# Performance work log

Measured on AMD Instinct MI355X. Metric: run time of the kernel, lower is better.

Reference implementation:

```python
import jax, jax.numpy as jnp
import numpy as np
import math

CHUNK = 128


def setup_inputs() -> dict:
    key = jax.random.key(0)
    ks = jax.random.split(key, 12)
    B, S, H, D = 2, 4096, 1024, 2048  # D = hidden_dim * expansion_factor
    std = 0.02
    inp = {
        "hidden_states": jax.random.normal(ks[0], (B, S, H), jnp.float32),
        "Wq": jax.random.normal(ks[1], (H, D), jnp.float32) * std,
        "bq": jnp.zeros((D,), jnp.float32),
        "Wk": jax.random.normal(ks[2], (H, D), jnp.float32) * std,
        "bk": jnp.zeros((D,), jnp.float32),
        "Wv": jax.random.normal(ks[3], (H, D), jnp.float32) * std,
        "bv": jnp.zeros((D,), jnp.float32),
        "Wg": jax.random.normal(ks[4], (H, D), jnp.float32) * std,
        "bg": jnp.zeros((D,), jnp.float32),
        "Wo": jax.random.normal(ks[5], (D, H), jnp.float32) * std,
        "bo": jnp.zeros((H,), jnp.float32),
    }
    return inp


def reference(hidden_states, Wq, bq, Wk, bk, Wv, bv, Wg, bg, Wo, bo):
    B, S, H = hidden_states.shape
    D = Wq.shape[1]
    cs = CHUNK
    nC = S // cs  # seq_len chosen as multiple of chunk_size (no padding path)

    q = hidden_states @ Wq + bq
    k = hidden_states @ Wk + bk
    v = hidden_states @ Wv + bv
    gate = jax.nn.sigmoid(hidden_states @ Wg + bg)

    qc = q.reshape(B, nC, cs, D)
    kc = k.reshape(B, nC, cs, D)
    vc = v.reshape(B, nC, cs, D)
    gc = gate.reshape(B, nC, cs, D)

    # intra-chunk causal softmax attention (vectorized over all chunks)
    scale = 1.0 / math.sqrt(D)
    attn = jnp.einsum('bncd,bnkd->bnck', qc, kc) * scale  # [B,nC,cs,cs]
    causal = jnp.tril(jnp.ones((cs, cs), bool))
    attn = jnp.where(causal, attn, -jnp.inf)
    attn = jax.nn.softmax(attn, axis=-1)
    local = jnp.einsum('bnck,bnkd->bncd', attn, vc)

    # inter-chunk linear-attention state accumulation:
    # cross_i = q_i @ sum_{j<i} K_j^T V_j  (sequential scan over chunks)
    def step(state, xs):
        qi, ki, vi = xs  # each [B,cs,D]
        cross = jnp.einsum('bcd,bde->bce', qi, state)
        state = state + jnp.einsum('bcd,bce->bde', ki, vi)
        return state, cross

    state0 = jnp.zeros((B, D, D), hidden_states.dtype)
    _, cross = jax.lax.scan(
        step, state0,
        (qc.transpose(1, 0, 2, 3), kc.transpose(1, 0, 2, 3), vc.transpose(1, 0, 2, 3)))
    cross = cross.transpose(1, 0, 2, 3)  # [B,nC,cs,D]

    out = (local + cross) * gc
    out = out.reshape(B, S, D)
    return out @ Wo + bo
```

## Files before the change

kernel.cpp:

```cpp
#include <hip/hip_runtime.h>
#include <hip/hip_bf16.h>
#include <math.h>


typedef __bf16 bf16_t;
typedef __bf16 bf16x8 __attribute__((ext_vector_type(8)));
typedef __bf16 bf16x4 __attribute__((ext_vector_type(4)));
typedef float f32x4 __attribute__((ext_vector_type(4)));

#define NB_ 2
#define SEQ 4096
#define HID 1024
#define DD 2048
#define BS 8192
#define LDS_BIG 73728
#define LDS_PAIR 49152

__device__ __forceinline__ void async16(const void* g, void* l) {
  __builtin_amdgcn_global_load_lds(
      (const __attribute__((address_space(1))) void*)g,
      (__attribute__((address_space(3))) void*)l, 16, 0, 0);
}

#define VMW0 asm volatile("s_waitcnt vmcnt(0)" ::: "memory")
#define BARR __builtin_amdgcn_s_barrier()
#define FEN asm volatile("" ::: "memory")

template <int WM, int WN>
__device__ __forceinline__ void coreTB(const bf16_t* __restrict__ A, int lda,
                                       const bf16_t* __restrict__ B, int ldb, int nt,
                                       bf16_t* lds, f32x4 (&acc)[4][4]) {
  constexpr int T = WM * WN * 64;
  constexpr int AE = WM * 64 * 32;
  constexpr int BUF = AE + WN * 64 * 32;
  constexpr int NISS = BUF / (T * 8);
  const int t = threadIdx.x;
  const int lane = t & 63, w = t >> 6;
  const int wm = w / WN, wn = w % WN;
  const int lr = lane & 15, lg = lane >> 4;

  int aOff[4], bOff[4];
#pragma unroll
  for (int f = 0; f < 4; ++f) {
    int ra = wm * 64 + f * 16 + lr;
    aOff[f] = ra * 32 + (((lg + (ra >> 1)) & 3) << 3);
    int rb = wn * 64 + f * 16 + lr;
    bOff[f] = AE + rb * 32 + (((lg + (rb >> 1)) & 3) << 3);
  }
  int src[NISS];
#pragma unroll
  for (int q = 0; q < NISS; ++q) {
    int e = q * T * 8 + t * 8;
    bool isB = (q * T * 8) >= AE;
    int e2 = isB ? e - AE : e;
    int r = e2 >> 5;
    int g = (((e2 >> 3) & 3) - (r >> 1)) & 3;
    src[q] = r * (isB ? ldb : lda) + g * 8;
  }
#pragma unroll
  for (int m = 0; m < 4; ++m)
#pragma unroll
    for (int n = 0; n < 4; ++n) acc[m][n] = (f32x4){0.f, 0.f, 0.f, 0.f};

#pragma unroll
  for (int q = 0; q < NISS; ++q) {
    bool isB = (q * T * 8) >= AE;
    async16((isB ? B : A) + src[q], lds + q * T * 8 + t * 8);
  }
  {
    const int k1 = (1 < nt ? 1 : 0) << 5;
#pragma unroll
    for (int q = 0; q < NISS; ++q) {
      bool isB = (q * T * 8) >= AE;
      async16((isB ? B : A) + k1 + src[q], lds + BUF + q * T * 8 + t * 8);
    }
  }

  for (int tt = 0; tt < nt; ++tt) {
    bf16_t* cur = lds + (tt % 3) * BUF;
    bf16_t* nxt = lds + ((tt + 2) % 3) * BUF;
    const int kn = (tt + 2 < nt ? tt + 2 : 0) << 5;
    if constexpr (NISS == 3) {
      asm volatile("s_waitcnt vmcnt(3)" ::: "memory");
    } else if constexpr (NISS == 4) {
      asm volatile("s_waitcnt vmcnt(4)" ::: "memory");
    } else {
      asm volatile("s_waitcnt vmcnt(0)" ::: "memory");
    }
    BARR; FEN;
    bf16x8 af[4], bv[4];
#pragma unroll
    for (int f = 0; f < 4; ++f) af[f] = *reinterpret_cast<const bf16x8*>(&cur[aOff[f]]);
#pragma unroll
    for (int f = 0; f < 4; ++f) bv[f] = *reinterpret_cast<const bf16x8*>(&cur[bOff[f]]);
#pragma unroll
    for (int q = 0; q < NISS; ++q) {
      bool isB = (q * T * 8) >= AE;
      async16((isB ? B : A) + kn + src[q], nxt + q * T * 8 + t * 8);
    }
    __builtin_amdgcn_s_setprio(1);
#pragma unroll
    for (int mf = 0; mf < 4; ++mf)
#pragma unroll
      for (int nf = 0; nf < 4; ++nf)
        acc[mf][nf] =
            __builtin_amdgcn_mfma_f32_16x16x32_bf16(af[mf], bv[nf], acc[mf][nf], 0, 0, 0);
    __builtin_amdgcn_s_setprio(0);
  }
  VMW0;
  BARR; FEN;
}

__global__ void k_cvt(const float4* __restrict__ in, bf16x4* __restrict__ out, int n4) {
  int i = blockIdx.x * blockDim.x + threadIdx.x;
  if (i < n4) {
    float4 v = in[i];
    bf16x4 o;
    o[0] = (bf16_t)v.x; o[1] = (bf16_t)v.y; o[2] = (bf16_t)v.z; o[3] = (bf16_t)v.w;
    out[i] = o;
  }
}

__global__ void k_tconv(const float* __restrict__ in, bf16_t* __restrict__ out,
                        int R, int C) {
  __shared__ bf16_t tile[64][65];
  int bc = blockIdx.x, br = blockIdx.y;
  int t = threadIdx.x;
  int c = t & 63, r0 = t >> 6;
#pragma unroll
  for (int rr = 0; rr < 64; rr += 4) {
    int r = rr + r0;
    tile[r][c] = (bf16_t)in[(long)(br * 64 + r) * C + bc * 64 + c];
  }
  __syncthreads();
#pragma unroll
  for (int rr = 0; rr < 64; rr += 4) {
    int r = rr + r0;
    out[(long)(bc * 64 + r) * R + br * 64 + c] = tile[c][r];
  }
}

__global__ __launch_bounds__(512, 4) void k_gemm_qkvg(
    const bf16_t* __restrict__ hsb, const bf16_t* __restrict__ Wt4,
    const float* __restrict__ bq, const float* __restrict__ bk,
    const float* __restrict__ bv, const float* __restrict__ bg,
    bf16_t* __restrict__ out, bf16_t* __restrict__ Vt) {
  extern __shared__ bf16_t lds[];
  const int SP = 136;
  const int SPT = 264;
  int i = blockIdx.x;
  int xcd = i & 7, g = i >> 3;
  int mb = g >> 3;
  int nb = xcd * 8 + (g & 7);
  f32x4 acc[4][4];
  coreTB<4, 2>(hsb + (long)mb * 256 * HID, HID, Wt4 + (long)nb * 128 * HID, HID,
               HID / 32, lds, acc);
  const int t = threadIdx.x, lane = t & 63, w = t >> 6;
  const int wm = w >> 1, wn = w & 1, lr = lane & 15, lg = lane >> 4;
  int z = nb >> 4;
  const float* bias = z == 0 ? bq : z == 1 ? bk : z == 2 ? bv : bg;
  int colT = (nb & 15) * 128;
  float b4[4];
#pragma unroll
  for (int nf = 0; nf < 4; ++nf) b4[nf] = bias[colT + wn * 64 + nf * 16 + lr];
  if (z != 2) {
#pragma unroll
    for (int mf = 0; mf < 4; ++mf)
#pragma unroll
      for (int reg = 0; reg < 4; ++reg) {
        int lrow = wm * 64 + mf * 16 + lg * 4 + reg;
#pragma unroll
        for (int nf = 0; nf < 4; ++nf) {
          float v = acc[mf][nf][reg] + b4[nf];
          if (z == 3) v = 1.f / (1.f + __expf(-v));
          lds[lrow * SP + wn * 64 + nf * 16 + lr] = (bf16_t)v;
        }
      }
    __syncthreads();
    bf16_t* O = out + (long)z * BS * DD + (long)mb * 256 * DD + colT;
#pragma unroll
    for (int it = 0; it < 8; ++it) {
      int s = it * 512 + t;
      int row = s >> 4, sg = s & 15;
      bf16x8 v = *reinterpret_cast<const bf16x8*>(&lds[row * SP + sg * 8]);
      *reinterpret_cast<bf16x8*>(&O[(long)row * DD + sg * 8]) = v;
    }
  } else {
#pragma unroll
    for (int mf = 0; mf < 4; ++mf)
#pragma unroll
      for (int reg = 0; reg < 4; ++reg) {
        int lrow = wm * 64 + mf * 16 + lg * 4 + reg;
#pragma unroll
        for (int nf = 0; nf < 4; ++nf) {
          int d = wn * 64 + nf * 16 + lr;
          lds[d * SPT + lrow] = (bf16_t)(acc[mf][nf][reg] + b4[nf]);
        }
      }
    __syncthreads();
    int bz = mb >> 4, smb = mb & 15;
    bf16_t* Vd = Vt + ((long)bz * DD + colT) * SEQ + smb * 256;
#pragma unroll
    for (int it = 0; it < 8; ++it) {
      int s = it * 512 + t;
      int d = s >> 5, sg = s & 31;
      bf16x8 v = *reinterpret_cast<const bf16x8*>(&lds[d * SPT + sg * 8]);
      *reinterpret_cast<bf16x8*>(&Vd[(long)d * SEQ + sg * 8]) = v;
    }
  }
}

__global__ __launch_bounds__(256, 3) void k_pair(const bf16_t* __restrict__ Q,
                                                 const bf16_t* __restrict__ Kb,
                                                 bf16_t* __restrict__ P) {
  extern __shared__ bf16_t lds[];
  const int SP = 136;
  int p = blockIdx.x, b = blockIdx.y;
  int c = 0, base = 0;
  while (base + c + 1 <= p) { base += c + 1; ++c; }
  int jt = p - base;
  f32x4 acc[4][4];
  coreTB<2, 2>(Q + ((long)b * SEQ + (long)c * 128) * DD, DD,
               Kb + ((long)b * SEQ + (long)jt * 128) * DD, DD, DD / 32, lds, acc);
  const int t = threadIdx.x, lane = t & 63, w = t >> 6;
  const int wm = w >> 1, wn = w & 1, lr = lane & 15, lg = lane >> 4;
  bf16_t* Pt = P + ((long)b * SEQ + (long)c * 128) * (long)SEQ + (long)jt * 128;
  const bool diag = (jt == c);
  const float scale = 0.02209708691207961f;
#pragma unroll
  for (int mf = 0; mf < 4; ++mf)
#pragma unroll
    for (int reg = 0; reg < 4; ++reg) {
      int row = wm * 64 + mf * 16 + lg * 4 + reg;
#pragma unroll
      for (int nf = 0; nf < 4; ++nf) {
        int col = wn * 64 + nf * 16 + lr;
        float v = acc[mf][nf][reg];
        if (diag) v = (col <= row) ? v * scale : -1e30f;
        lds[row * SP + col] = (bf16_t)v;
      }
    }
  __syncthreads();
  if (diag) {
    if (t < 128) {
      int r = t;
      bf16_t* rowp = lds + r * SP;
      float mx = -1e30f;
      for (int cc = 0; cc <= r; ++cc) mx = fmaxf(mx, (float)rowp[cc]);
      float ssum = 0.f;
      for (int cc = 0; cc <= r; ++cc) ssum += __expf((float)rowp[cc] - mx);
      float inv = 1.f / ssum;
      for (int cc = 0; cc < 128; ++cc) {
        float v = (cc <= r) ? __expf((float)rowp[cc] - mx) * inv : 0.f;
        rowp[cc] = (bf16_t)v;
      }
    }
    __syncthreads();
  }
#pragma unroll
  for (int it = 0; it < 8; ++it) {
    int s = it * 256 + t;
    int row = s >> 4, sg = s & 15;
    bf16x8 v = *reinterpret_cast<const bf16x8*>(&lds[row * SP + sg * 8]);
    *reinterpret_cast<bf16x8*>(&Pt[(long)row * SEQ + sg * 8]) = v;
  }
  if (diag && !(c & 1)) {
    bf16x8 zv = {};
#pragma unroll
    for (int it = 0; it < 8; ++it) {
      int s = it * 256 + t;
      int row = s >> 4, sg = s & 15;
      *reinterpret_cast<bf16x8*>(&Pt[(long)row * SEQ + 128 + sg * 8]) = zv;
    }
  }
}

__global__ __launch_bounds__(512, 4) void k_gemm2(const bf16_t* __restrict__ P,
                                                  const bf16_t* __restrict__ Vt,
                                                  const bf16_t* __restrict__ G,
                                                  bf16_t* __restrict__ OutPre) {
  extern __shared__ bf16_t lds[];
  const int SP = 136;
  int bid = blockIdx.x;
  int ip = 15 - (bid >> 5);
  int r2 = bid & 31;
  int nb = r2 >> 1, b2 = r2 & 1;
  f32x4 acc[4][4];
  coreTB<4, 2>(P + ((long)b2 * SEQ + (long)ip * 256) * (long)SEQ, SEQ,
               Vt + (long)b2 * DD * SEQ + (long)nb * 128 * SEQ, SEQ, (ip + 1) * 8,
               lds, acc);
  const int t = threadIdx.x, lane = t & 63, w = t >> 6;
  const int wm = w >> 1, wn = w & 1, lr = lane & 15, lg = lane >> 4;
  long rowb = (long)b2 * SEQ + (long)ip * 256;
#pragma unroll
  for (int mf = 0; mf < 4; ++mf)
#pragma unroll
    for (int reg = 0; reg < 4; ++reg) {
      int lrow = wm * 64 + mf * 16 + lg * 4 + reg;
#pragma unroll
      for (int nf = 0; nf < 4; ++nf) {
        int col = wn * 64 + nf * 16 + lr;
        float gg = (float)G[(rowb + lrow) * DD + nb * 128 + col];
        lds[lrow * SP + col] = (bf16_t)(acc[mf][nf][reg] * gg);
      }
    }
  __syncthreads();
  bf16_t* O = OutPre + rowb * DD + nb * 128;
#pragma unroll
  for (int it = 0; it < 8; ++it) {
    int s = it * 512 + t;
    int row = s >> 4, sg = s & 15;
    bf16x8 v = *reinterpret_cast<const bf16x8*>(&lds[row * SP + sg * 8]);
    *reinterpret_cast<bf16x8*>(&O[(long)row * DD + sg * 8]) = v;
  }
}

__global__ __launch_bounds__(512, 4) void k_gemm3(const bf16_t* __restrict__ OutPre,
                                                  const bf16_t* __restrict__ Wot,
                                                  const float* __restrict__ bo,
                                                  float* __restrict__ out) {
  extern __shared__ bf16_t lds[];
  int mb = blockIdx.x >> 2, nb = blockIdx.x & 3;
  f32x4 acc[4][4];
  coreTB<2, 4>(OutPre + (long)mb * 128 * DD, DD, Wot + (long)nb * 256 * DD, DD,
               DD / 32, lds, acc);
  const int t = threadIdx.x, lane = t & 63, w = t >> 6;
  const int wm = w >> 2, wn = w & 3, lr = lane & 15, lg = lane >> 4;
  int colbase = nb * 256 + wn * 64;
  float b4[4];
#pragma unroll
  for (int nf = 0; nf < 4; ++nf) b4[nf] = bo[colbase + nf * 16 + lr];
#pragma unroll
  for (int mf = 0; mf < 4; ++mf)
#pragma unroll
    for (int reg = 0; reg < 4; ++reg) {
      long row = mb * 128 + wm * 64 + mf * 16 + lg * 4 + reg;
#pragma unroll
      for (int nf = 0; nf < 4; ++nf)
        out[row * HID + colbase + nf * 16 + lr] = acc[mf][nf][reg] + b4[nf];
    }
}

extern "C" void kernel_launch(void* const* d_in, const int* in_sizes, int n_in,
                              void* d_out, int out_size, void* d_ws, size_t ws_size,
                              hipStream_t stream) {
  const float* hs = (const float*)d_in[0];
  const float* Wq = (const float*)d_in[1];
  const float* bq = (const float*)d_in[2];
  const float* Wk = (const float*)d_in[3];
  const float* bk = (const float*)d_in[4];
  const float* Wv = (const float*)d_in[5];
  const float* bv = (const float*)d_in[6];
  const float* Wg = (const float*)d_in[7];
  const float* bg = (const float*)d_in[8];
  const float* Wo = (const float*)d_in[9];
  const float* bo = (const float*)d_in[10];
  float* out = (float*)d_out;

  char* ws = (char*)d_ws;
  const size_t MB = 1024 * 1024;
  bf16_t* P = (bf16_t*)(ws);
  bf16_t* hsb = (bf16_t*)(ws);
  bf16_t* Wt4 = (bf16_t*)(ws + 16 * MB);
  bf16_t* Wot = (bf16_t*)(ws + 64 * MB);
  bf16_t* QKVG = (bf16_t*)(ws + 68 * MB);
  bf16_t* Vt = (bf16_t*)(ws + 196 * MB);

  bf16_t* Qb = QKVG;
  bf16_t* Kbuf = QKVG + (long)BS * DD;
  bf16_t* Vbuf = QKVG + 2l * BS * DD;
  bf16_t* Gbuf = QKVG + 3l * BS * DD;
  bf16_t* OutPre = Vbuf;

  hipFuncSetAttribute((const void*)k_gemm_qkvg,
                      hipFuncAttributeMaxDynamicSharedMemorySize, LDS_BIG);
  hipFuncSetAttribute((const void*)k_pair,
                      hipFuncAttributeMaxDynamicSharedMemorySize, LDS_PAIR);
  hipFuncSetAttribute((const void*)k_gemm2,
                      hipFuncAttributeMaxDynamicSharedMemorySize, LDS_BIG);
  hipFuncSetAttribute((const void*)k_gemm3,
                      hipFuncAttributeMaxDynamicSharedMemorySize, LDS_BIG);

  k_cvt<<<(BS * HID / 4 + 255) / 256, 256, 0, stream>>>((const float4*)hs,
                                                        (bf16x4*)hsb, BS * HID / 4);
  k_tconv<<<dim3(DD / 64, HID / 64), 256, 0, stream>>>(Wq, Wt4 + 0l * DD * HID, HID, DD);
  k_tconv<<<dim3(DD / 64, HID / 64), 256, 0, stream>>>(Wk, Wt4 + 1l * DD * HID, HID, DD);
  k_tconv<<<dim3(DD / 64, HID / 64), 256, 0, stream>>>(Wv, Wt4 + 2l * DD * HID, HID, DD);
  k_tconv<<<dim3(DD / 64, HID / 64), 256, 0, stream>>>(Wg, Wt4 + 3l * DD * HID, HID, DD);
  k_tconv<<<dim3(HID / 64, DD / 64), 256, 0, stream>>>(Wo, Wot, DD, HID);

  k_gemm_qkvg<<<2048, 512, LDS_BIG, stream>>>(hsb, Wt4, bq, bk, bv, bg, QKVG, Vt);

  k_pair<<<dim3(528, 2), 256, LDS_PAIR, stream>>>(Qb, Kbuf, P);

  k_gemm2<<<512, 512, LDS_BIG, stream>>>(P, Vt, Gbuf, OutPre);

  k_gemm3<<<256, 512, LDS_BIG, stream>>>(OutPre, Wot, bo, out);
}
```

Before: 433.5 us.

## Retile pair and output GEMMs to 128x256, fuse weight transposes

k_pair now computes 128x256 score tiles with 512 threads, so it launches 272 blocks instead of 528. It writes non-diagonal tiles straight to global memory and runs the diagonal softmax from an fp32 LDS buffer with a rotated index. k_gemm2 switches to 128x256 tiles and writes the gated result directly, without staging it in LDS. The four QKVG weight transposes are merged into one launch. The direct global stores are scattered 2-byte writes rather than coalesced 16-byte vectors, which may cost bandwidth. The diagonal softmax also still runs on a single 128-thread serial loop.

Result: faster. 424.7 us (-2.0%).

```diff
diff --git a/kernel.cpp b/kernel.cpp
--- a/kernel.cpp
+++ b/kernel.cpp
@@ -13,8 +13,7 @@
 #define HID 1024
 #define DD 2048
 #define BS 8192
-#define LDS_BIG 73728
-#define LDS_PAIR 49152
+#define LDS_TB 73728
 
 __device__ __forceinline__ void async16(const void* g, void* l) {
   __builtin_amdgcn_global_load_lds(
@@ -118,6 +117,29 @@
     bf16x4 o;
     o[0] = (bf16_t)v.x; o[1] = (bf16_t)v.y; o[2] = (bf16_t)v.z; o[3] = (bf16_t)v.w;
     out[i] = o;
+  }
+}
+
+__global__ void k_tconv4(const float* __restrict__ W0, const float* __restrict__ W1,
+                         const float* __restrict__ W2, const float* __restrict__ W3,
+                         bf16_t* __restrict__ out) {
+  __shared__ bf16_t tile[64][65];
+  int z = blockIdx.z;
+  const float* in = z == 0 ? W0 : z == 1 ? W1 : z == 2 ? W2 : W3;
+  bf16_t* o = out + (long)z * DD * HID;
+  int bc = blockIdx.x, br = blockIdx.y;
+  int t = threadIdx.x;
+  int c = t & 63, r0 = t >> 6;
+#pragma unroll
+  for (int rr = 0; rr < 64; rr += 4) {
+    int r = rr + r0;
+    tile[r][c] = (bf16_t)in[(long)(br * 64 + r) * DD + bc * 64 + c];
+  }
+  __syncthreads();
+#pragma unroll
+  for (int rr = 0; rr < 64; rr += 4) {
+    int r = rr + r0;
+    o[(long)(bc * 64 + r) * HID + br * 64 + c] = tile[c][r];
   }
 }
 
@@ -210,23 +232,24 @@
   }
 }
 
-__global__ __launch_bounds__(256, 3) void k_pair(const bf16_t* __restrict__ Q,
+__global__ __launch_bounds__(512, 4) void k_pair(const bf16_t* __restrict__ Q,
                                                  const bf16_t* __restrict__ Kb,
                                                  bf16_t* __restrict__ P) {
   extern __shared__ bf16_t lds[];
-  const int SP = 136;
   int p = blockIdx.x, b = blockIdx.y;
   int c = 0, base = 0;
-  while (base + c + 1 <= p) { base += c + 1; ++c; }
+  while (base + (c >> 1) + 1 <= p) { base += (c >> 1) + 1; ++c; }
   int jt = p - base;
   f32x4 acc[4][4];
-  coreTB<2, 2>(Q + ((long)b * SEQ + (long)c * 128) * DD, DD,
-               Kb + ((long)b * SEQ + (long)jt * 128) * DD, DD, DD / 32, lds, acc);
+  coreTB<2, 4>(Q + ((long)b * SEQ + (long)c * 128) * DD, DD,
+               Kb + ((long)b * SEQ + (long)jt * 256) * DD, DD, DD / 32, lds, acc);
   const int t = threadIdx.x, lane = t & 63, w = t >> 6;
-  const int wm = w >> 1, wn = w & 1, lr = lane & 15, lg = lane >> 4;
-  bf16_t* Pt = P + ((long)b * SEQ + (long)c * 128) * (long)SEQ + (long)jt * 128;
-  const bool diag = (jt == c);
+  const int wm = w >> 2, wn = w & 3, lr = lane & 15, lg = lane >> 4;
+  bf16_t* Pt = P + ((long)b * SEQ + (long)c * 128) * (long)SEQ + (long)jt * 256;
+  const bool hasDiag = (jt == (c >> 1));
+  const int side = c & 1;
   const float scale = 0.02209708691207961f;
+  float* smf = (float*)lds;
 #pragma unroll
   for (int mf = 0; mf < 4; ++mf)
 #pragma unroll
@@ -236,41 +259,29 @@
       for (int nf = 0; nf < 4; ++nf) {
         int col = wn * 64 + nf * 16 + lr;
         float v = acc[mf][nf][reg];
-        if (diag) v = (col <= row) ? v * scale : -1e30f;
-        lds[row * SP + col] = (bf16_t)v;
-      }
-    }
-  __syncthreads();
-  if (diag) {
+        if (hasDiag && ((col >> 7) == side)) {
+          int cc = col & 127;
+          float sv = v * scale;
+          smf[row * 128 + ((cc + row) & 127)] = (cc <= row) ? sv : -1e30f;
+        } else {
+          if (hasDiag && side == 0 && (col >> 7) == 1) v = 0.f;
+          Pt[(long)row * SEQ + col] = (bf16_t)v;
+        }
+      }
+    }
+  if (hasDiag) {
+    __syncthreads();
     if (t < 128) {
       int r = t;
-      bf16_t* rowp = lds + r * SP;
       float mx = -1e30f;
-      for (int cc = 0; cc <= r; ++cc) mx = fmaxf(mx, (float)rowp[cc]);
-      float ssum = 0.f;
-      for (int cc = 0; cc <= r; ++cc) ssum += __expf((float)rowp[cc] - mx);
-      float inv = 1.f / ssum;
+      for (int cc = 0; cc <= r; ++cc) mx = fmaxf(mx, smf[r * 128 + ((cc + r) & 127)]);
+      float s = 0.f;
+      for (int cc = 0; cc <= r; ++cc) s += __expf(smf[r * 128 + ((cc + r) & 127)] - mx);
+      float inv = 1.f / s;
       for (int cc = 0; cc < 128; ++cc) {
-        float v = (cc <= r) ? __expf((float)rowp[cc] - mx) * inv : 0.f;
-        rowp[cc] = (bf16_t)v;
-      }
-    }
-    __syncthreads();
-  }
-#pragma unroll
-  for (int it = 0; it < 8; ++it) {
-    int s = it * 256 + t;
-    int row = s >> 4, sg = s & 15;
-    bf16x8 v = *reinterpret_cast<const bf16x8*>(&lds[row * SP + sg * 8]);
-    *reinterpret_cast<bf16x8*>(&Pt[(long)row * SEQ + sg * 8]) = v;
-  }
-  if (diag && !(c & 1)) {
-    bf16x8 zv = {};
-#pragma unroll
-    for (int it = 0; it < 8; ++it) {
-      int s = it * 256 + t;
-      int row = s >> 4, sg = s & 15;
-      *reinterpret_cast<bf16x8*>(&Pt[(long)row * SEQ + 128 + sg * 8]) = zv;
+        float v = (cc <= r) ? __expf(smf[r * 128 + ((cc + r) & 127)] - mx) * inv : 0.f;
+        Pt[(long)r * SEQ + side * 128 + cc] = (bf16_t)v;
+      }
     }
   }
 }
@@ -280,39 +291,28 @@
                                                   const bf16_t* __restrict__ G,
                                                   bf16_t* __restrict__ OutPre) {
   extern __shared__ bf16_t lds[];
-  const int SP = 136;
   int bid = blockIdx.x;
-  int ip = 15 - (bid >> 5);
-  int r2 = bid & 31;
-  int nb = r2 >> 1, b2 = r2 & 1;
+  int mq = 31 - (bid >> 4);
+  int r2 = bid & 15;
+  int nb = r2 >> 1, b = r2 & 1;
   f32x4 acc[4][4];
-  coreTB<4, 2>(P + ((long)b2 * SEQ + (long)ip * 256) * (long)SEQ, SEQ,
-               Vt + (long)b2 * DD * SEQ + (long)nb * 128 * SEQ, SEQ, (ip + 1) * 8,
+  coreTB<2, 4>(P + ((long)b * SEQ + (long)mq * 128) * (long)SEQ, SEQ,
+               Vt + (long)b * DD * SEQ + (long)nb * 256 * SEQ, SEQ, (mq + 1) * 4,
                lds, acc);
   const int t = threadIdx.x, lane = t & 63, w = t >> 6;
-  const int wm = w >> 1, wn = w & 1, lr = lane & 15, lg = lane >> 4;
-  long rowb = (long)b2 * SEQ + (long)ip * 256;
+  const int wm = w >> 2, wn = w & 3, lr = lane & 15, lg = lane >> 4;
 #pragma unroll
   for (int mf = 0; mf < 4; ++mf)
 #pragma unroll
     for (int reg = 0; reg < 4; ++reg) {
-      int lrow = wm * 64 + mf * 16 + lg * 4 + reg;
+      long row = (long)b * SEQ + (long)mq * 128 + wm * 64 + mf * 16 + lg * 4 + reg;
 #pragma unroll
       for (int nf = 0; nf < 4; ++nf) {
-        int col = wn * 64 + nf * 16 + lr;
-        float gg = (float)G[(rowb + lrow) * DD + nb * 128 + col];
-        lds[lrow * SP + col] = (bf16_t)(acc[mf][nf][reg] * gg);
-      }
-    }
-  __syncthreads();
-  bf16_t* O = OutPre + rowb * DD + nb * 128;
-#pragma unroll
-  for (int it = 0; it < 8; ++it) {
-    int s = it * 512 + t;
-    int row = s >> 4, sg = s & 15;
-    bf16x8 v = *reinterpret_cast<const bf16x8*>(&lds[row * SP + sg * 8]);
-    *reinterpret_cast<bf16x8*>(&O[(long)row * DD + sg * 8]) = v;
-  }
+        long idx = row * DD + nb * 256 + wn * 64 + nf * 16 + lr;
+        float g = (float)G[idx];
+        OutPre[idx] = (bf16_t)(acc[mf][nf][reg] * g);
+      }
+    }
 }
 
 __global__ __launch_bounds__(512, 4) void k_gemm3(const bf16_t* __restrict__ OutPre,
@@ -373,27 +373,24 @@
   bf16_t* OutPre = Vbuf;
 
   hipFuncSetAttribute((const void*)k_gemm_qkvg,
-                      hipFuncAttributeMaxDynamicSharedMemorySize, LDS_BIG);
+                      hipFuncAttributeMaxDynamicSharedMemorySize, LDS_TB);
   hipFuncSetAttribute((const void*)k_pair,
-                      hipFuncAttributeMaxDynamicSharedMemorySize, LDS_PAIR);
+                      hipFuncAttributeMaxDynamicSharedMemorySize, LDS_TB);
   hipFuncSetAttribute((const void*)k_gemm2,
-                      hipFuncAttributeMaxDynamicSharedMemorySize, LDS_BIG);
+                      hipFuncAttributeMaxDynamicSharedMemorySize, LDS_TB);
   hipFuncSetAttribute((const void*)k_gemm3,
-                      hipFuncAttributeMaxDynamicSharedMemorySize, LDS_BIG);
+                      hipFuncAttributeMaxDynamicSharedMemorySize, LDS_TB);
 
   k_cvt<<<(BS * HID / 4 + 255) / 256, 256, 0, stream>>>((const float4*)hs,
                                                         (bf16x4*)hsb, BS * HID / 4);
-  k_tconv<<<dim3(DD / 64, HID / 64), 256, 0, stream>>>(Wq, Wt4 + 0l * DD * HID, HID, DD);
-  k_tconv<<<dim3(DD / 64, HID / 64), 256, 0, stream>>>(Wk, Wt4 + 1l * DD * HID, HID, DD);
-  k_tconv<<<dim3(DD / 64, HID / 64), 256, 0, stream>>>(Wv, Wt4 + 2l * DD * HID, HID, DD);
-  k_tconv<<<dim3(DD / 64, HID / 64), 256, 0, stream>>>(Wg, Wt4 + 3l * DD * HID, HID, DD);
+  k_tconv4<<<dim3(DD / 64, HID / 64, 4), 256, 0, stream>>>(Wq, Wk, Wv, Wg, Wt4);
   k_tconv<<<dim3(HID / 64, DD / 64), 256, 0, stream>>>(Wo, Wot, DD, HID);
 
-  k_gemm_qkvg<<<2048, 512, LDS_BIG, stream>>>(hsb, Wt4, bq, bk, bv, bg, QKVG, Vt);
-
-  k_pair<<<dim3(528, 2), 256, LDS_PAIR, stream>>>(Qb, Kbuf, P);
-
-  k_gemm2<<<512, 512, LDS_BIG, stream>>>(P, Vt, Gbuf, OutPre);
-
-  k_gemm3<<<256, 512, LDS_BIG, stream>>>(OutPre, Wot, bo, out);
-}
+  k_gemm_qkvg<<<2048, 512, LDS_TB, stream>>>(hsb, Wt4, bq, bk, bv, bg, QKVG, Vt);
+
+  k_pair<<<dim3(272, 2), 512, LDS_TB, stream>>>(Qb, Kbuf, P);
+
+  k_gemm2<<<512, 512, LDS_TB, stream>>>(P, Vt, Gbuf, OutPre);
+
+  k_gemm3<<<256, 512, LDS_TB, stream>>>(OutPre, Wot, bo, out);
+}
```
